# Kernel optimization log

Measured on AMD Instinct MI355X. Metric: run time of the kernel, lower is better.

Reference implementation:

```python
import jax, jax.numpy as jnp
import numpy as np

THR_CONF = 0.5   # threshold_conf
THR_NMS = 0.3    # threshold_nms
K = 1024         # fixed pre-NMS top-k per image (jit-friendly stand-in for boolean filter)
VAR0, VAR1 = 0.1, 0.2  # SSD/RetinaFace decode variances


def setup_inputs() -> dict:
    key = jax.random.key(0)
    k1, k2, k3, k4 = jax.random.split(key, 4)
    B, N = 64, 16800
    p_loc = jax.random.normal(k1, (B, N, 4), jnp.float32)
    p_conf = jax.random.normal(k2, (B, N, 1), jnp.float32)
    p_landms = jax.random.normal(k3, (B, N, 10), jnp.float32)
    # anchor priors in cxcywh, normalized coords
    anchors = jax.random.uniform(k4, (N, 4), jnp.float32, 0.05, 0.6)
    return {"p_loc": p_loc, "p_conf": p_conf, "p_landms": p_landms, "anchors": anchors}


def _decode_boxes(anchors, loc):
    # fix_bbox: cxcy = a_cxcy + loc_xy * var0 * a_wh ; wh = a_wh * exp(loc_wh * var1)
    xy = anchors[..., :2] + loc[..., :2] * VAR0 * anchors[..., 2:]
    wh = anchors[..., 2:] * jnp.exp(loc[..., 2:] * VAR1)
    # xywh2ltrb
    return jnp.concatenate([xy - wh * 0.5, xy + wh * 0.5], axis=-1)  # (B,N,4)


def _decode_kpts(anchors, landms):
    # fix_keypoints: 5 points, each = a_cxcy + d * var0 * a_wh
    B, N, _ = landms.shape
    pts = landms.reshape(B, N, 5, 2)
    kp = anchors[:, None, :2] + pts * VAR0 * anchors[:, None, 2:]
    return kp.reshape(B, N, 10)


def _iou_matrix(b):  # b: (K,4) ltrb -> (K,K)
    area = jnp.maximum(b[:, 2] - b[:, 0], 0.0) * jnp.maximum(b[:, 3] - b[:, 1], 0.0)
    lt = jnp.maximum(b[:, None, :2], b[None, :, :2])
    rb = jnp.minimum(b[:, None, 2:], b[None, :, 2:])
    wh = jnp.maximum(rb - lt, 0.0)
    inter = wh[..., 0] * wh[..., 1]
    return inter / (area[:, None] + area[None, :] - inter + 1e-9)


def _nms_one(boxes, kpts, scores):
    # boxes (N,4), kpts (N,10), scores (N,)
    s = jnp.where(scores >= THR_CONF, scores, -1.0)  # conf mask
    vals, idx = jax.lax.top_k(s, K)                  # sorted candidates (torch nms sorts by score)
    b = boxes[idx]
    kp = kpts[idx]
    iou = _iou_matrix(b)
    ar = jnp.arange(K)

    def body(suppressed, i):
        keep_i = (vals[i] >= THR_CONF) & (~suppressed[i])
        suppressed = suppressed | (keep_i & (iou[i] > THR_NMS) & (ar > i))
        return suppressed, keep_i

    _, keep = jax.lax.scan(body, jnp.zeros(K, dtype=bool), ar)
    m = keep.astype(b.dtype)[:, None]
    # (K,15) = ltrb(4) | keypoints(10) | score(1), zeroed where suppressed/filtered
    return jnp.concatenate([b, kp, vals[:, None]], axis=-1) * m


def reference(p_loc, p_conf, p_landms, anchors):
    scores = jax.nn.sigmoid(p_conf)[..., 0]       # (B,N)
    boxes = _decode_boxes(anchors, p_loc)         # (B,N,4) ltrb
    kpts = _decode_kpts(anchors, p_landms)        # (B,N,10)
    return jax.vmap(_nms_one)(boxes, kpts, scores)  # (B,K,15)
```

## Files before the change

### kernel.cpp

```cpp
#include <hip/hip_runtime.h>
#include <cmath>

#define NB 64
#define NN 16800
#define KK 1024
#define NT 1024
#define CAP 2048
#define RQ 17

typedef unsigned long long ull;

__device__ __forceinline__ ull score_key_d(float cf) {
  double s = 1.0 / (1.0 + exp(-(double)cf));
  if (!(s >= 0.5)) return 0ull;
  return ((ull)__double_as_longlong(s) & 0xFFFFFFFFFFFFFull) + 1ull;
}

__device__ __forceinline__ void decode_box_d(const float* lp, const float* ap,
                                             double& X0, double& Y0,
                                             double& X1, double& Y1,
                                             double& AR) {
#pragma clang fp contract(off)
  double l0 = (double)lp[0], l1 = (double)lp[1];
  double l2 = (double)lp[2], l3 = (double)lp[3];
  double a0 = (double)ap[0], a1 = (double)ap[1];
  double a2 = (double)ap[2], a3 = (double)ap[3];
  double xy0 = a0 + (l0 * 0.1) * a2;
  double xy1 = a1 + (l1 * 0.1) * a3;
  double w = a2 * exp(l2 * 0.2);
  double h = a3 * exp(l3 * 0.2);
  X0 = xy0 - w * 0.5; Y0 = xy1 - h * 0.5;
  X1 = xy0 + w * 0.5; Y1 = xy1 + h * 0.5;
  AR = fmax(X1 - X0, 0.0) * fmax(Y1 - Y0, 0.0);
}

__device__ __forceinline__ bool iou_gt_d(double i0, double i1, double i2,
                                         double i3, double ia, double j0,
                                         double j1, double j2, double j3,
                                         double ja) {
#pragma clang fp contract(off)
  double lt0 = fmax(i0, j0), lt1 = fmax(i1, j1);
  double rb0 = fmin(i2, j2), rb1 = fmin(i3, j3);
  double w0 = fmax(rb0 - lt0, 0.0), w1 = fmax(rb1 - lt1, 0.0);
  double inter = w0 * w1;
  double den = ((ia + ja) - inter) + 1e-9;
  return (inter / den) > 0.3;
}

__device__ __forceinline__ float rdlanef(float v, int l) {
  return __uint_as_float(__builtin_amdgcn_readlane(__float_as_uint(v), l));
}

__device__ __forceinline__ ull readlane64(ull v, int l) {
  unsigned int lo = __builtin_amdgcn_readlane((unsigned int)v, l);
  unsigned int hi = __builtin_amdgcn_readlane((unsigned int)(v >> 32), l);
  return ((ull)hi << 32) | (ull)lo;
}

__global__ __launch_bounds__(1024, 1) void sort_kernel(
    const float* __restrict__ p_loc, const float* __restrict__ p_conf,
    const float* __restrict__ anchors, unsigned int* __restrict__ sidx_s,
    float* __restrict__ fbox, float* __restrict__ sval) {
  const int b = blockIdx.x;
  const int tid = threadIdx.x;
  const int lane = tid & 63;
  const int wave = tid >> 6;

  __shared__ ull skey[CAP];
  __shared__ unsigned int sidx[CAP];
  __shared__ unsigned int hist[4096];
  __shared__ unsigned int base[4096];
  __shared__ unsigned int totals[64], chcarry[64];
  __shared__ unsigned int sh_found, sh_binT, sh_cB;
  __shared__ unsigned int scnt, sh_digit, sh_r, sh_c;

  ull rkey[RQ];
  {
    const float* conf = p_conf + (size_t)b * NN;
    #pragma unroll
    for (int q = 0; q < RQ; ++q) {
      const int i = tid + q * NT;
      rkey[q] = (i < NN) ? score_key_d(conf[i]) : 0ull;
    }
  }

  for (int i = tid; i < 4096; i += NT) hist[i] = 0u;
  if (tid == 0) sh_found = 0u;
  __syncthreads();
  #pragma unroll
  for (int q = 0; q < RQ; ++q) {
    ull k = rkey[q];
    if (k != 0ull) {
      unsigned int bin = (unsigned int)(k >> 40);
      if (bin > 4095u) bin = 4095u;
      atomicAdd(&hist[bin], 1u);
    }
  }
  __syncthreads();
  for (int chunk = wave; chunk < 64; chunk += 16) {
    const int bin = chunk * 64 + (63 - lane);
    unsigned int c0 = hist[bin];
    unsigned int x = c0;
    #pragma unroll
    for (int d = 1; d < 64; d <<= 1) {
      unsigned int y = __shfl_up(x, d);
      if (lane >= d) x += y;
    }
    base[bin] = x;
    if (lane == 63) totals[chunk] = x;
  }
  __syncthreads();
  if (wave == 0) {
    const int chunk = 63 - lane;
    unsigned int t0 = totals[chunk];
    unsigned int x = t0;
    #pragma unroll
    for (int d = 1; d < 64; d <<= 1) {
      unsigned int y = __shfl_up(x, d);
      if (lane >= d) x += y;
    }
    chcarry[chunk] = x - t0;
  }
  __syncthreads();
  for (int chunk = wave; chunk < 64; chunk += 16) {
    const int bin = chunk * 64 + (63 - lane);
    unsigned int c0 = hist[bin];
    unsigned int S = chcarry[chunk] + base[bin] - c0;
    base[bin] = S;
    if (S < (unsigned)KK && (unsigned)KK <= S + c0) {
      sh_found = 1u; sh_binT = (unsigned int)bin; sh_cB = c0;
    }
  }
  __syncthreads();
  const bool fastOK = (sh_found != 0u) && (sh_cB <= 64u);
  const unsigned int binT = sh_binT;

  if (fastOK) {
    for (int i = tid; i < KK + 64; i += NT) { skey[i] = 0ull; sidx[i] = 0xFFFFFFFFu; }
    __syncthreads();
    #pragma unroll
    for (int q = 0; q < RQ; ++q) {
      const int i = tid + q * NT;
      ull k = rkey[q];
      if (k != 0ull) {
        unsigned int bin = (unsigned int)(k >> 40);
        if (bin > 4095u) bin = 4095u;
        if (bin >= binT) {
          unsigned int pos = atomicAdd(&base[bin], 1u);
          if (pos < (unsigned)(KK + 64)) { skey[pos] = k; sidx[pos] = (unsigned int)i; }
        }
      }
    }
    __syncthreads();
    for (int bin = (int)binT + tid; bin < 4096; bin += NT) {
      unsigned int cnt = hist[bin];
      if (cnt >= 2u) {
        int hi2 = (int)base[bin];
        int lo2 = hi2 - (int)cnt;
        for (int m2 = lo2 + 1; m2 < hi2; ++m2) {
          ull kx = skey[m2]; unsigned int ix = sidx[m2];
          int n2 = m2;
          while (n2 > lo2) {
            ull kp = skey[n2 - 1]; unsigned int ip = sidx[n2 - 1];
            bool after = (kp < kx) || (kp == kx && ip > ix);
            if (!after) break;
            skey[n2] = kp; sidx[n2] = ip; --n2;
          }
          skey[n2] = kx; sidx[n2] = ix;
        }
      }
    }
    __syncthreads();
  } else {
    unsigned int r = KK;
    ull prefix = 0ull, T = 0ull;
    for (int pass = 0; pass < 7; ++pass) {
      const int shift = 48 - pass * 8;
      if (tid < 256) hist[tid] = 0u;
      __syncthreads();
      const ull pm = pass ? ~((1ull << (shift + 8)) - 1ull) : 0ull;
      #pragma unroll
      for (int q = 0; q < RQ; ++q) {
        ull k = rkey[q];
        if (k != 0ull && (k & pm) == prefix)
          atomicAdd(&hist[(unsigned int)(k >> shift) & 255u], 1u);
      }
      __syncthreads();
      if (wave == 0) {
        if (lane == 0) { sh_digit = 0u; sh_r = r; sh_c = 0u; }
        unsigned int carry = 0;
        for (int chunk = 3; chunk >= 0; --chunk) {
          const int bin = chunk * 64 + (63 - lane);
          unsigned int c = hist[bin];
          unsigned int x = c;
          #pragma unroll
          for (int d = 1; d < 64; d <<= 1) {
            unsigned int y = __shfl_up(x, d);
            if (lane >= d) x += y;
          }
          unsigned int excl = x - c;
          unsigned int S = carry + excl;
          bool hit = (S < r) && (r <= S + c);
          ull bal = __ballot(hit ? 1 : 0);
          if (bal != 0ull) {
            int hl = __ffsll((long long)bal) - 1;
            unsigned int Sf = __shfl(S, hl);
            unsigned int bf = __shfl((unsigned int)bin, hl);
            unsigned int cf = __shfl(c, hl);
            if (lane == 0) { sh_digit = bf; sh_r = r - Sf; sh_c = cf; }
            break;
          }
          carry += __shfl(x, 63);
        }
      }
      __syncthreads();
      prefix |= ((ull)sh_digit << shift);
      r = sh_r;
      const unsigned int cntge = (KK - r) + sh_c;
      if (cntge <= CAP || pass == 6) { T = prefix; break; }
    }

    if (tid == 0) scnt = 0u;
    for (int i = tid; i < CAP; i += NT) { skey[i] = 0ull; sidx[i] = 0xFFFFFFFFu; }
    __syncthreads();
    #pragma unroll
    for (int q = 0; q < RQ; ++q) {
      const int i = tid + q * NT;
      ull k = rkey[q];
      if (k != 0ull && k >= T) {
        unsigned int pos = atomicAdd(&scnt, 1u);
        if (pos < CAP) { skey[pos] = k; sidx[pos] = (unsigned int)i; }
      }
    }
    __syncthreads();

    for (unsigned int k2 = 2; k2 <= CAP; k2 <<= 1) {
      for (unsigned int j = k2 >> 1; j > 0; j >>= 1) {
        for (int i = tid; i < CAP; i += NT) {
          int ixj = i ^ (int)j;
          if (ixj > i) {
            bool up = ((i & k2) == 0);
            ull ka = skey[i], kbv = skey[ixj];
            unsigned int ia = sidx[i], ib = sidx[ixj];
            bool a_after_b = (ka < kbv) || (ka == kbv && ia > ib);
            if (a_after_b == up) {
              skey[i] = kbv; skey[ixj] = ka;
              sidx[i] = ib; sidx[ixj] = ia;
            }
          }
        }
        __syncthreads();
      }
    }
  }

  const ull mykey = skey[tid];
  const unsigned int myidx = sidx[tid];
  double X0 = 0.0, Y0 = 0.0, X1 = 0.0, Y1 = 0.0, AR = 0.0;
  float v = -1.0f;
  if (mykey != 0ull) {
    decode_box_d(p_loc + ((size_t)b * NN + myidx) * 4,
                 anchors + (size_t)myidx * 4, X0, Y0, X1, Y1, AR);
    double s = __longlong_as_double(
        (long long)(0x3FE0000000000000ull | (mykey - 1ull)));
    v = (float)s;
  }
  sidx_s[(size_t)b * KK + tid] = myidx;
  float* fb = fbox + (size_t)b * 5 * KK;
  fb[0 * KK + tid] = (float)X0; fb[1 * KK + tid] = (float)Y0;
  fb[2 * KK + tid] = (float)X1; fb[3 * KK + tid] = (float)Y1;
  fb[4 * KK + tid] = (float)AR;
  sval[(size_t)b * KK + tid] = v;
}

__global__ __launch_bounds__(256) void pair_kernel(
    const float* __restrict__ p_loc, const float* __restrict__ anchors,
    const unsigned int* __restrict__ sidx_s, const float* __restrict__ fbox,
    const float* __restrict__ sval, ull* __restrict__ maskg) {
  const int img = blockIdx.x;
  const int wave = threadIdx.x >> 6;
  const int lane = threadIdx.x & 63;
  const int t = blockIdx.y * 4 + wave;

  int rg = 0, rem = t;
  while (rem >= 16 - rg) { rem -= 16 - rg; ++rg; }
  const int cg = rg + rem;

  const float* fb = fbox + (size_t)img * 5 * KK;
  const int irow = rg * 64 + lane;
  const int jcol = cg * 64 + lane;

  float r0 = fb[0 * KK + irow], r1 = fb[1 * KK + irow];
  float r2 = fb[2 * KK + irow], r3 = fb[3 * KK + irow];
  float ra = fb[4 * KK + irow];
  unsigned int ri = sidx_s[(size_t)img * KK + irow];

  const float cj0 = fb[0 * KK + jcol], cj1 = fb[1 * KK + jcol];
  const float cj2 = fb[2 * KK + jcol], cj3 = fb[3 * KK + jcol];
  const float caj = fb[4 * KK + jcol];
  const unsigned int cidx = sidx_s[(size_t)img * KK + jcol];

  unsigned int wlo = 0u, whi = 0u;

  #pragma unroll 8
  for (int rr = 0; rr < 64; ++rr) {
    const float bi0 = rdlanef(r0, rr), bi1 = rdlanef(r1, rr);
    const float bi2 = rdlanef(r2, rr), bi3 = rdlanef(r3, rr);
    const float ai = rdlanef(ra, rr);
    float lt0 = fmaxf(bi0, cj0), lt1 = fmaxf(bi1, cj1);
    float q0 = fminf(bi2, cj2), q1 = fminf(bi3, cj3);
    float w0 = fmaxf(q0 - lt0, 0.0f), w1 = fmaxf(q1 - lt1, 0.0f);
    float inter = w0 * w1;
    float den = ((ai + caj) - inter) + 1e-9f;
    float d = inter - 0.3f * den;
    bool bit = d > 0.0f;
    bool unc = fabsf(d) <= den * 1e-3f;
    if (__builtin_expect((bool)__ballot(unc ? 1 : 0), 0)) {
      const unsigned int rbi = __builtin_amdgcn_readlane(ri, rr);
      if (unc) {
        double rX0, rY0, rX1, rY1, rAR, qX0, qY0, qX1, qY1, qAR;
        decode_box_d(p_loc + ((size_t)img * NN + rbi) * 4,
                     anchors + (size_t)rbi * 4, rX0, rY0, rX1, rY1, rAR);
        decode_box_d(p_loc + ((size_t)img * NN + cidx) * 4,
                     anchors + (size_t)cidx * 4, qX0, qY0, qX1, qY1, qAR);
        bit = iou_gt_d(rX0, rY0, rX1, rY1, rAR, qX0, qY0, qX1, qY1, qAR);
      }
    }
    bit = bit && (jcol > rg * 64 + rr);
    ull m = __ballot(bit ? 1 : 0);
    const bool mine = (lane == rr);
    wlo = mine ? (unsigned int)m : wlo;
    whi = mine ? (unsigned int)(m >> 32) : whi;
  }

  maskg[((size_t)img * KK + (size_t)rg * 64 + lane) * 16 + cg] =
      ((ull)whi << 32) | (ull)wlo;
}

__global__ __launch_bounds__(1024, 1) void resolve_kernel(
    const float* __restrict__ p_landms, const float* __restrict__ anchors,
    const unsigned int* __restrict__ sidx_s, const float* __restrict__ fbox,
    const float* __restrict__ sval, const ull* __restrict__ maskg,
    float* __restrict__ out) {
  const int img = blockIdx.x, tid = threadIdx.x, lane = tid & 63,
            wave = tid >> 6;
  __shared__ ull buf[2][2048];
  __shared__ float svbuf[KK];
  __shared__ ull keepw[16];
  const ull* mg = maskg + (size_t)img * KK * 16;

  svbuf[tid] = sval[(size_t)img * KK + tid];
  for (int u = tid; u < 2048; u += NT) buf[0][u] = mg[u];
  __syncthreads();

  ull supw = 0ull;
  for (int s = 0; s < 8; ++s) {
    const int cur = s & 1;
    if (wave != 0) {
      if (s + 1 < 8) {
        const ull* src = mg + (size_t)(s + 1) * 2048;
        const int wmin = 2 * (s + 1);
        for (int u = tid - 64; u < 2048; u += NT - 64)
          if ((u & 15) >= wmin) buf[cur ^ 1][u] = src[u];
      }
    } else {
      #pragma unroll
      for (int half = 0; half < 2; ++half) {
        const int g = 2 * s + half;
        const ull vm = __ballot(svbuf[g * 64 + lane] >= 0.0f);
        ull curw = readlane64(supw, g);
        ull km = 0ull;
        #pragma unroll 8
        for (int rr = 0; rr < 64; ++rr) {
          const int rl = half * 64 + rr;
          ull mw = 0ull;
          if (lane < 16 && lane >= g) mw = buf[cur][rl * 16 + lane];
          const bool keep = (((vm >> rr) & 1ull) != 0ull) &&
                            (((curw >> rr) & 1ull) == 0ull);
          if (keep) {
            km |= (1ull << rr);
            supw |= mw;
            curw |= readlane64(mw, g);
          }
        }
        if (lane == 0) keepw[g] = km;
      }
    }
    __syncthreads();
  }

  const bool keep = ((keepw[tid >> 6] >> (tid & 63)) & 1ull) != 0ull;
  float* op = out + ((size_t)img * KK + tid) * 15;
  if (keep) {
    const float* fb = fbox + (size_t)img * 5 * KK;
    op[0] = fb[0 * KK + tid]; op[1] = fb[1 * KK + tid];
    op[2] = fb[2 * KK + tid]; op[3] = fb[3 * KK + tid];
    const unsigned int myidx = sidx_s[(size_t)img * KK + tid];
    const float* pp = p_landms + ((size_t)img * NN + myidx) * 10;
    const float* ap = anchors + (size_t)myidx * 4;
    double a0 = (double)ap[0], a1 = (double)ap[1];
    double a2 = (double)ap[2], a3 = (double)ap[3];
    #pragma unroll
    for (int q = 0; q < 5; ++q) {
      double px = (double)pp[2 * q], py = (double)pp[2 * q + 1];
      op[4 + 2 * q]     = (float)(a0 + (px * 0.1) * a2);
      op[4 + 2 * q + 1] = (float)(a1 + (py * 0.1) * a3);
    }
    op[14] = svbuf[tid];
  } else {
    #pragma unroll
    for (int q = 0; q < 15; ++q) op[q] = 0.0f;
  }
}

__global__ __launch_bounds__(1024, 1) void fallback_kernel(
    const float* __restrict__ p_loc, const float* __restrict__ p_conf,
    const float* __restrict__ p_landms, const float* __restrict__ anchors,
    const ull* __restrict__ gkeys, float* __restrict__ out) {
  const int b = blockIdx.x;
  const int tid = threadIdx.x;
  const int lane = tid & 63;
  const int wave = tid >> 6;

  __shared__ ull skey[CAP];
  __shared__ unsigned int sidx[CAP];
  __shared__ float fb0[KK], fb1[KK], fb2[KK], fb3[KK], farr[KK];
  __shared__ float svalf[KK];
  __shared__ ull chunkmask[32][16];
  __shared__ unsigned int keepm[32];
  __shared__ ull supShared[16];
  __shared__ unsigned int hist[256];
  __shared__ unsigned int scnt, sh_digit, sh_r;

  unsigned long long rkey[RQ];
  if (gkeys != nullptr) {
    const ull* kb = gkeys + (size_t)b * NN;
    #pragma unroll
    for (int q = 0; q < RQ; ++q) {
      const int i = tid + q * NT;
      rkey[q] = (i < NN) ? kb[i] : 0ull;
    }
  } else {
    const float* conf = p_conf + (size_t)b * NN;
    #pragma unroll
    for (int q = 0; q < RQ; ++q) {
      const int i = tid + q * NT;
      rkey[q] = (i < NN) ? score_key_d(conf[i]) : 0ull;
    }
  }

  unsigned int r = KK;
  ull prefix = 0ull;
  for (int pass = 0; pass < 7; ++pass) {
    const int shift = 48 - pass * 8;
    if (tid < 256) hist[tid] = 0u;
    __syncthreads();
    const ull pm = (pass == 0) ? 0ull : ~((1ull << (shift + 8)) - 1ull);
    #pragma unroll
    for (int q = 0; q < RQ; ++q) {
      const int i = tid + q * NT;
      if (i < NN) {
        ull k = rkey[q];
        if (k != 0ull && (k & pm) == prefix)
          atomicAdd(&hist[(unsigned int)(k >> shift) & 255u], 1u);
      }
    }
    __syncthreads();
    if (wave == 0) {
      if (lane == 0) { sh_digit = 0u; sh_r = r; }
      unsigned int carry = 0;
      for (int chunk = 3; chunk >= 0; --chunk) {
        const int bin = chunk * 64 + (63 - lane);
        unsigned int c = hist[bin];
        unsigned int x = c;
        #pragma unroll
        for (int d = 1; d < 64; d <<= 1) {
          unsigned int y = __shfl_up(x, d);
          if (lane >= d) x += y;
        }
        unsigned int excl = x - c;
        unsigned int S = carry + excl;
        bool hit = (S < r) && (r <= S + c);
        ull bal = __ballot(hit ? 1 : 0);
        if (bal != 0ull) {
          int hl = __ffsll((long long)bal) - 1;
          unsigned int Sf = __shfl(S, hl);
          unsigned int bf = __shfl((unsigned int)bin, hl);
          if (lane == 0) { sh_digit = bf; sh_r = r - Sf; }
          break;
        }
        carry += __shfl(x, 63);
      }
    }
    __syncthreads();
    prefix |= ((ull)sh_digit << shift);
    r = sh_r;
    __syncthreads();
  }
  const ull T = prefix;

  if (tid == 0) scnt = 0u;
  for (int i = tid; i < CAP; i += NT) { skey[i] = 0ull; sidx[i] = 0xFFFFFFFFu; }
  __syncthreads();
  #pragma unroll
  for (int q = 0; q < RQ; ++q) {
    const int i = tid + q * NT;
    if (i < NN) {
      ull k = rkey[q];
      if (k != 0ull && k >= T) {
        unsigned int pos = atomicAdd(&scnt, 1u);
        if (pos < CAP) { skey[pos] = k; sidx[pos] = (unsigned int)i; }
      }
    }
  }
  __syncthreads();

  for (unsigned int k2 = 2; k2 <= CAP; k2 <<= 1) {
    for (unsigned int j = k2 >> 1; j > 0; j >>= 1) {
      for (int i = tid; i < CAP; i += NT) {
        int ixj = i ^ (int)j;
        if (ixj > i) {
          bool up = ((i & k2) == 0);
          ull ka = skey[i], kb = skey[ixj];
          unsigned int ia = sidx[i], ib = sidx[ixj];
          bool a_after_b = (ka < kb) || (ka == kb && ia > ib);
          if (a_after_b == up) {
            skey[i] = kb; skey[ixj] = ka;
            sidx[i] = ib; sidx[ixj] = ia;
          }
        }
      }
      __syncthreads();
    }
  }

  const ull mykey = skey[tid];
  const unsigned int myidx = sidx[tid];
  double dX0 = 0.0, dY0 = 0.0, dX1 = 0.0, dY1 = 0.0, dAR = 0.0;
  {
    float v = -1.0f;
    if (mykey != 0ull) {
      decode_box_d(p_loc + ((size_t)b * NN + myidx) * 4,
                   anchors + (size_t)myidx * 4, dX0, dY0, dX1, dY1, dAR);
      double s = __longlong_as_double(
          (long long)(0x3FE0000000000000ull | (mykey - 1ull)));
      v = (float)s;
    }
    fb0[tid] = (float)dX0; fb1[tid] = (float)dY0;
    fb2[tid] = (float)dX1; fb3[tid] = (float)dY1;
    farr[tid] = (float)dAR;
    svalf[tid] = v;
  }
  if (tid < 16) supShared[tid] = 0ull;
  if (tid < 32) keepm[tid] = 0u;
  __syncthreads();

  const float cj0 = fb0[tid], cj1 = fb1[tid], cj2 = fb2[tid], cj3 = fb3[tid];
  const float caj = farr[tid];
  ull supw = 0ull;

  for (int c = 0; c < 32; ++c) {
    for (int rr = 0; rr < 32; ++rr) {
      const int i = c * 32 + rr;
      const bool rowDead =
          (svalf[i] < 0.0f) ||
          (((supShared[i >> 6] >> (i & 63)) & 1ull) != 0ull);
      if (rowDead) continue;
      float bi0 = fb0[i], bi1 = fb1[i], bi2 = fb2[i], bi3 = fb3[i];
      float ai = farr[i];
      float lt0 = fmaxf(bi0, cj0), lt1 = fmaxf(bi1, cj1);
      float q0 = fminf(bi2, cj2), q1 = fminf(bi3, cj3);
      float w0 = fmaxf(q0 - lt0, 0.0f), w1 = fmaxf(q1 - lt1, 0.0f);
      float inter = w0 * w1;
      float den = ((ai + caj) - inter) + 1e-9f;
      float d = inter - 0.3f * den;
      bool bit = d > 0.0f;
      bool unc = fabsf(d) <= den * 1e-3f;
      if (__builtin_expect((bool)__ballot(unc ? 1 : 0), 0)) {
        if (unc) {
          const unsigned int ridx = sidx[i];
          double rX0, rY0, rX1, rY1, rAR;
          decode_box_d(p_loc + ((size_t)b * NN + ridx) * 4,
                       anchors + (size_t)ridx * 4, rX0, rY0, rX1, rY1, rAR);
          bit = iou_gt_d(rX0, rY0, rX1, rY1, rAR, dX0, dY0, dX1, dY1, dAR);
        }
      }
      bit = bit && (tid > i);
      ull m = __ballot(bit ? 1 : 0);
      if (lane == 0) chunkmask[rr][wave] = m;
    }
    __syncthreads();
    if (wave == 0) {
      unsigned int km = 0u;
      for (int rr = 0; rr < 32; ++rr) {
        const int i = c * 32 + rr;
        ull sc = __shfl(supw, i >> 6);
        bool keep = (svalf[i] >= 0.0f) && (((sc >> (i & 63)) & 1ull) == 0ull);
        if (keep) {
          km |= (1u << rr);
          if (lane < 16) supw |= chunkmask[rr][lane];
        }
      }
      if (lane == 0) keepm[c] = km;
      if (lane < 16) supShared[lane] = supw;
    }
    __syncthreads();
  }

  {
    const bool keep = ((keepm[tid >> 5] >> (tid & 31)) & 1u) != 0u;
    float* op = out + ((size_t)b * KK + tid) * 15;
    if (keep) {
      op[0] = fb0[tid]; op[1] = fb1[tid]; op[2] = fb2[tid]; op[3] = fb3[tid];
      const float* pp = p_landms + ((size_t)b * NN + myidx) * 10;
      const float* ap = anchors + (size_t)myidx * 4;
      double a0 = (double)ap[0], a1 = (double)ap[1];
      double a2 = (double)ap[2], a3 = (double)ap[3];
      #pragma unroll
      for (int q = 0; q < 5; ++q) {
        double px = (double)pp[2 * q], py = (double)pp[2 * q + 1];
        op[4 + 2 * q]     = (float)(a0 + (px * 0.1) * a2);
        op[4 + 2 * q + 1] = (float)(a1 + (py * 0.1) * a3);
      }
      op[14] = svalf[tid];
    } else {
      #pragma unroll
      for (int q = 0; q < 15; ++q) op[q] = 0.0f;
    }
  }
}

extern "C" void kernel_launch(void* const* d_in, const int* in_sizes, int n_in,
                              void* d_out, int out_size, void* d_ws, size_t ws_size,
                              hipStream_t stream) {
  const float* p_loc    = (const float*)d_in[0];
  const float* p_conf   = (const float*)d_in[1];
  const float* p_landms = (const float*)d_in[2];
  const float* anchors  = (const float*)d_in[3];
  float* out = (float*)d_out;
  (void)in_sizes; (void)n_in; (void)out_size;

  const size_t off_sidx = 0;
  const size_t off_fbox = off_sidx + (size_t)NB * KK * 4;
  const size_t off_sval = off_fbox + (size_t)NB * 5 * KK * 4;
  const size_t off_mask = off_sval + (size_t)NB * KK * 4;
  const size_t mask_bytes = (size_t)NB * KK * 16 * sizeof(ull);
  const size_t total = off_mask + mask_bytes;

  char* ws = (char*)d_ws;

  if (ws_size >= total) {
    unsigned int* sidx_s = (unsigned int*)(ws + off_sidx);
    float* fbox = (float*)(ws + off_fbox);
    float* sval = (float*)(ws + off_sval);
    ull* maskg = (ull*)(ws + off_mask);

    hipLaunchKernelGGL(sort_kernel, dim3(NB), dim3(NT), 0, stream,
                       p_loc, p_conf, anchors, sidx_s, fbox, sval);
    hipLaunchKernelGGL(pair_kernel, dim3(NB, 34), dim3(256), 0, stream,
                       p_loc, anchors, sidx_s, fbox, sval, maskg);
    hipLaunchKernelGGL(resolve_kernel, dim3(NB), dim3(NT), 0, stream,
                       p_landms, anchors, sidx_s, fbox, sval, maskg, out);
  } else {
    hipLaunchKernelGGL(fallback_kernel, dim3(NB), dim3(NT), 0, stream,
                       p_loc, p_conf, p_landms, anchors, (const ull*)nullptr,
                       out);
  }
}
```

Measured before the change: 222.0 us.

## Rank scores by raw float logit bits and load row boxes as scalars

The sort kernel now builds 32-bit keys straight from the raw confidence logits (sigmoid is monotonic, and threshold 0.5 maps to logit >= 0) instead of computing a double-precision sigmoid per element. It bins by logit value, halves the key storage in shared memory, and cuts the radix fallback from 7 passes to 4. The sigmoid is computed only for the 1024 survivors. The pair kernel also reads the row boxes through wave-uniform pointers, so they become scalar loads instead of per-iteration readlane operations. A risk is that ties between distinct logits that round to the same double sigmoid are now ordered differently, and the new histogram binning may change how often the fast path is taken.

```diff
diff --git a/kernel.cpp b/kernel.cpp
--- a/kernel.cpp
+++ b/kernel.cpp
@@ -9,6 +9,17 @@
 #define RQ 17
 
 typedef unsigned long long ull;
+
+__device__ __forceinline__ unsigned int score_key_f(float cf) {
+  if (!(cf >= 0.0f)) return 0u;
+  return (__float_as_uint(cf) & 0x7FFFFFFFu) + 1u;
+}
+
+__device__ __forceinline__ unsigned int bin_of_key(unsigned int key) {
+  float cf = __uint_as_float(key - 1u);
+  unsigned int bi = (unsigned int)(int)(cf * 1024.0f);
+  return bi > 4095u ? 4095u : bi;
+}
 
 __device__ __forceinline__ ull score_key_d(float cf) {
   double s = 1.0 / (1.0 + exp(-(double)cf));
@@ -66,7 +77,7 @@
   const int lane = tid & 63;
   const int wave = tid >> 6;
 
-  __shared__ ull skey[CAP];
+  __shared__ unsigned int skey[CAP];
   __shared__ unsigned int sidx[CAP];
   __shared__ unsigned int hist[4096];
   __shared__ unsigned int base[4096];
@@ -74,14 +85,13 @@
   __shared__ unsigned int sh_found, sh_binT, sh_cB;
   __shared__ unsigned int scnt, sh_digit, sh_r, sh_c;
 
-  ull rkey[RQ];
-  {
-    const float* conf = p_conf + (size_t)b * NN;
-    #pragma unroll
-    for (int q = 0; q < RQ; ++q) {
-      const int i = tid + q * NT;
-      rkey[q] = (i < NN) ? score_key_d(conf[i]) : 0ull;
-    }
+  const float* conf = p_conf + (size_t)b * NN;
+
+  unsigned int rkey[RQ];
+  #pragma unroll
+  for (int q = 0; q < RQ; ++q) {
+    const int i = tid + q * NT;
+    rkey[q] = (i < NN) ? score_key_f(conf[i]) : 0u;
   }
 
   for (int i = tid; i < 4096; i += NT) hist[i] = 0u;
@@ -89,12 +99,8 @@
   __syncthreads();
   #pragma unroll
   for (int q = 0; q < RQ; ++q) {
-    ull k = rkey[q];
-    if (k != 0ull) {
-      unsigned int bin = (unsigned int)(k >> 40);
-      if (bin > 4095u) bin = 4095u;
-      atomicAdd(&hist[bin], 1u);
-    }
+    unsigned int k = rkey[q];
+    if (k != 0u) atomicAdd(&hist[bin_of_key(k)], 1u);
   }
   __syncthreads();
   for (int chunk = wave; chunk < 64; chunk += 16) {
@@ -136,15 +142,14 @@
   const unsigned int binT = sh_binT;
 
   if (fastOK) {
-    for (int i = tid; i < KK + 64; i += NT) { skey[i] = 0ull; sidx[i] = 0xFFFFFFFFu; }
+    for (int i = tid; i < KK + 64; i += NT) { skey[i] = 0u; sidx[i] = 0xFFFFFFFFu; }
     __syncthreads();
     #pragma unroll
     for (int q = 0; q < RQ; ++q) {
       const int i = tid + q * NT;
-      ull k = rkey[q];
-      if (k != 0ull) {
-        unsigned int bin = (unsigned int)(k >> 40);
-        if (bin > 4095u) bin = 4095u;
+      unsigned int k = rkey[q];
+      if (k != 0u) {
+        unsigned int bin = bin_of_key(k);
         if (bin >= binT) {
           unsigned int pos = atomicAdd(&base[bin], 1u);
           if (pos < (unsigned)(KK + 64)) { skey[pos] = k; sidx[pos] = (unsigned int)i; }
@@ -158,10 +163,10 @@
         int hi2 = (int)base[bin];
         int lo2 = hi2 - (int)cnt;
         for (int m2 = lo2 + 1; m2 < hi2; ++m2) {
-          ull kx = skey[m2]; unsigned int ix = sidx[m2];
+          unsigned int kx = skey[m2]; unsigned int ix = sidx[m2];
           int n2 = m2;
           while (n2 > lo2) {
-            ull kp = skey[n2 - 1]; unsigned int ip = sidx[n2 - 1];
+            unsigned int kp = skey[n2 - 1]; unsigned int ip = sidx[n2 - 1];
             bool after = (kp < kx) || (kp == kx && ip > ix);
             if (!after) break;
             skey[n2] = kp; sidx[n2] = ip; --n2;
@@ -173,17 +178,17 @@
     __syncthreads();
   } else {
     unsigned int r = KK;
-    ull prefix = 0ull, T = 0ull;
-    for (int pass = 0; pass < 7; ++pass) {
-      const int shift = 48 - pass * 8;
+    unsigned int prefix = 0u, T = 0u;
+    for (int pass = 0; pass < 4; ++pass) {
+      const int shift = 24 - pass * 8;
       if (tid < 256) hist[tid] = 0u;
       __syncthreads();
-      const ull pm = pass ? ~((1ull << (shift + 8)) - 1ull) : 0ull;
+      const unsigned int pm = pass ? ~((1u << (shift + 8)) - 1u) : 0u;
       #pragma unroll
       for (int q = 0; q < RQ; ++q) {
-        ull k = rkey[q];
-        if (k != 0ull && (k & pm) == prefix)
-          atomicAdd(&hist[(unsigned int)(k >> shift) & 255u], 1u);
+        unsigned int k = rkey[q];
+        if (k != 0u && (k & pm) == prefix)
+          atomicAdd(&hist[(k >> shift) & 255u], 1u);
       }
       __syncthreads();
       if (wave == 0) {
@@ -206,28 +211,28 @@
             int hl = __ffsll((long long)bal) - 1;
             unsigned int Sf = __shfl(S, hl);
             unsigned int bf = __shfl((unsigned int)bin, hl);
-            unsigned int cf = __shfl(c, hl);
-            if (lane == 0) { sh_digit = bf; sh_r = r - Sf; sh_c = cf; }
+            unsigned int cf2 = __shfl(c, hl);
+            if (lane == 0) { sh_digit = bf; sh_r = r - Sf; sh_c = cf2; }
             break;
           }
           carry += __shfl(x, 63);
         }
       }
       __syncthreads();
-      prefix |= ((ull)sh_digit << shift);
+      prefix |= (sh_digit << shift);
       r = sh_r;
       const unsigned int cntge = (KK - r) + sh_c;
-      if (cntge <= CAP || pass == 6) { T = prefix; break; }
+      if (cntge <= CAP || pass == 3) { T = prefix; break; }
     }
 
     if (tid == 0) scnt = 0u;
-    for (int i = tid; i < CAP; i += NT) { skey[i] = 0ull; sidx[i] = 0xFFFFFFFFu; }
+    for (int i = tid; i < CAP; i += NT) { skey[i] = 0u; sidx[i] = 0xFFFFFFFFu; }
     __syncthreads();
     #pragma unroll
     for (int q = 0; q < RQ; ++q) {
       const int i = tid + q * NT;
-      ull k = rkey[q];
-      if (k != 0ull && k >= T) {
+      unsigned int k = rkey[q];
+      if (k != 0u && k >= T) {
         unsigned int pos = atomicAdd(&scnt, 1u);
         if (pos < CAP) { skey[pos] = k; sidx[pos] = (unsigned int)i; }
       }
@@ -240,7 +245,7 @@
           int ixj = i ^ (int)j;
           if (ixj > i) {
             bool up = ((i & k2) == 0);
-            ull ka = skey[i], kbv = skey[ixj];
+            unsigned int ka = skey[i], kbv = skey[ixj];
             unsigned int ia = sidx[i], ib = sidx[ixj];
             bool a_after_b = (ka < kbv) || (ka == kbv && ia > ib);
             if (a_after_b == up) {
@@ -254,15 +259,14 @@
     }
   }
 
-  const ull mykey = skey[tid];
+  const unsigned int mykey = skey[tid];
   const unsigned int myidx = sidx[tid];
   double X0 = 0.0, Y0 = 0.0, X1 = 0.0, Y1 = 0.0, AR = 0.0;
   float v = -1.0f;
-  if (mykey != 0ull) {
+  if (mykey != 0u) {
     decode_box_d(p_loc + ((size_t)b * NN + myidx) * 4,
                  anchors + (size_t)myidx * 4, X0, Y0, X1, Y1, AR);
-    double s = __longlong_as_double(
-        (long long)(0x3FE0000000000000ull | (mykey - 1ull)));
+    double s = 1.0 / (1.0 + exp(-(double)conf[myidx]));
     v = (float)s;
   }
   sidx_s[(size_t)b * KK + tid] = myidx;
@@ -286,13 +290,18 @@
   while (rem >= 16 - rg) { rem -= 16 - rg; ++rg; }
   const int cg = rg + rem;
 
+  const int rgs = __builtin_amdgcn_readfirstlane(rg);
+
   const float* fb = fbox + (size_t)img * 5 * KK;
-  const int irow = rg * 64 + lane;
+  const int irow = rgs * 64 + lane;
   const int jcol = cg * 64 + lane;
 
-  float r0 = fb[0 * KK + irow], r1 = fb[1 * KK + irow];
-  float r2 = fb[2 * KK + irow], r3 = fb[3 * KK + irow];
-  float ra = fb[4 * KK + irow];
+  const float* rb0 = fb + 0 * KK + rgs * 64;
+  const float* rb1 = fb + 1 * KK + rgs * 64;
+  const float* rb2 = fb + 2 * KK + rgs * 64;
+  const float* rb3 = fb + 3 * KK + rgs * 64;
+  const float* rba = fb + 4 * KK + rgs * 64;
+
   unsigned int ri = sidx_s[(size_t)img * KK + irow];
 
   const float cj0 = fb[0 * KK + jcol], cj1 = fb[1 * KK + jcol];
@@ -304,9 +313,9 @@
 
   #pragma unroll 8
   for (int rr = 0; rr < 64; ++rr) {
-    const float bi0 = rdlanef(r0, rr), bi1 = rdlanef(r1, rr);
-    const float bi2 = rdlanef(r2, rr), bi3 = rdlanef(r3, rr);
-    const float ai = rdlanef(ra, rr);
+    const float bi0 = rb0[rr], bi1 = rb1[rr];
+    const float bi2 = rb2[rr], bi3 = rb3[rr];
+    const float ai = rba[rr];
     float lt0 = fmaxf(bi0, cj0), lt1 = fmaxf(bi1, cj1);
     float q0 = fminf(bi2, cj2), q1 = fminf(bi3, cj3);
     float w0 = fmaxf(q0 - lt0, 0.0f), w1 = fmaxf(q1 - lt1, 0.0f);
@@ -326,14 +335,14 @@
         bit = iou_gt_d(rX0, rY0, rX1, rY1, rAR, qX0, qY0, qX1, qY1, qAR);
       }
     }
-    bit = bit && (jcol > rg * 64 + rr);
+    bit = bit && (jcol > rgs * 64 + rr);
     ull m = __ballot(bit ? 1 : 0);
     const bool mine = (lane == rr);
     wlo = mine ? (unsigned int)m : wlo;
     whi = mine ? (unsigned int)(m >> 32) : whi;
   }
 
-  maskg[((size_t)img * KK + (size_t)rg * 64 + lane) * 16 + cg] =
+  maskg[((size_t)img * KK + (size_t)rgs * 64 + lane) * 16 + cg] =
       ((ull)whi << 32) | (ull)wlo;
 }
 
```

Result: faster. 207.5 us (-6.5%).
